# Performance work log

Hardware: AMD Instinct MI355X
Metric: run time of the kernel (lower is better)

Reference implementation:

```python
import jax, jax.numpy as jnp
import numpy as np

INTERVAL = 0.5  # voxel_size_ratio
N_RAYS = 131072
M_SAMPLES = 8388608  # ~64 samples per ray on average
ALPHA_INIT = 0.01


def setup_inputs() -> dict:
    key = jax.random.key(0)
    k1, k2, k3 = jax.random.split(key, 3)
    density = jax.random.normal(k1, (M_SAMPLES,), jnp.float32)
    rgb_feat = jax.random.normal(k2, (M_SAMPLES, 3), jnp.float32)  # raw k0 colors
    # act_shift buffer: log(1/(1-alpha_init) - 1)
    shift = jnp.array([np.log(1.0 / (1.0 - ALPHA_INIT) - 1.0)], jnp.float32)
    # sorted ray ids (samples along each ray are contiguous, near->far)
    ray_id = jnp.sort(jax.random.randint(k3, (M_SAMPLES,), 0, N_RAYS)).astype(jnp.int32)
    return {"density": density, "rgb_feat": rgb_feat, "shift": shift,
            "ray_id": ray_id, "N": N_RAYS}


def reference(density, rgb_feat, shift, ray_id, N):
    # Raw2Alpha: alpha = 1 - (1 + exp(density + shift))^(-interval)
    #          = 1 - exp(-softplus(density + shift) * interval)
    sp = jax.nn.softplus(density + shift[0])
    log1ma = -sp * INTERVAL            # log(1 - alpha), exact
    alpha = 1.0 - jnp.exp(log1ma)

    # Alphas2Weights: per-ray exclusive cumulative product of (1 - alpha)
    # done in log space with a segmented exclusive cumsum.
    seg_tot = jax.ops.segment_sum(log1ma, ray_id, num_segments=N)   # [N] log prod per ray
    seg_excl = jnp.cumsum(seg_tot) - seg_tot                        # log prod of previous rays
    within_excl = jnp.cumsum(log1ma) - log1ma - seg_excl[ray_id]    # exclusive within segment
    T = jnp.exp(within_excl)          # transmittance before each sample
    weights = alpha * T               # [M]
    alphainv_last = jnp.exp(seg_tot)  # [N] leftover transmittance per ray

    # composite colors per ray + white-ish background via alphainv_last
    rgb = jax.nn.sigmoid(rgb_feat)
    rgb_marched = jax.ops.segment_sum(weights[:, None] * rgb, ray_id, num_segments=N)
    out = rgb_marched + alphainv_last[:, None]   # [N, 3]
    return weights, alphainv_last, out
```

## Files before the change

kernel.cpp:

```cpp
#include <hip/hip_runtime.h>

#define INTERVAL 0.5f

__device__ __forceinline__ float cheap_softplus(float x) {
    float e = __expf(-fabsf(x));
    return fmaxf(x, 0.0f) + __logf(1.0f + e);
}

__device__ __forceinline__ float fast_sigmoid(float x) {
    return 1.0f / (1.0f + __expf(-x));
}

#define DPP_ADD(x, ctrl, rmask)                                               \
    do {                                                                      \
        int _s = __builtin_amdgcn_update_dpp(0, __float_as_int(x), (ctrl),    \
                                             (rmask), 0xf, true);             \
        (x) += __int_as_float(_s);                                            \
    } while (0)

__device__ __forceinline__ float wave_inclusive_scan(float x) {
    DPP_ADD(x, 0x111, 0xf);
    DPP_ADD(x, 0x112, 0xf);
    DPP_ADD(x, 0x114, 0xf);
    DPP_ADD(x, 0x118, 0xf);
    DPP_ADD(x, 0x142, 0xa);
    DPP_ADD(x, 0x143, 0xc);
    return x;
}

__device__ __forceinline__ float bcast_lane63(float x) {
    return __int_as_float(__builtin_amdgcn_readlane(__float_as_int(x), 63));
}

__global__ __launch_bounds__(256) void seg_starts_kernel(
    const int* __restrict__ ray_id, int M, int N, int* __restrict__ starts)
{
    const int i = blockIdx.x * blockDim.x + threadIdx.x;
    if (i >= M) return;
    const int cur  = ray_id[i];
    const int prev = (i == 0) ? -1 : ray_id[i - 1];
    for (int r = prev + 1; r <= cur; ++r) starts[r] = i;
    if (i == M - 1) {
        for (int r = cur + 1; r <= N; ++r) starts[r] = M;
    }
}

__global__ __launch_bounds__(256) void favor_render_kernel(
    const float* __restrict__ density,
    const float* __restrict__ rgb_feat,
    const float* __restrict__ shift,
    const int*   __restrict__ starts,
    int M, int N,
    float* __restrict__ weights,
    float* __restrict__ alphainv_last,
    float* __restrict__ out3)
{
    const int wave = (blockIdx.x * blockDim.x + threadIdx.x) >> 6;
    const int t    = threadIdx.x & 63;
    if (wave >= N) return;
    const int ray = wave;

    const int start = starts[ray];
    const int end   = starts[ray + 1];

    const float sh = shift[0];

    float carry = 0.0f;
    float acc0 = 0.0f, acc1 = 0.0f, acc2 = 0.0f;

    for (int base = start; base < end; base += 128) {
        const int i0 = base + t;
        const int i1 = i0 + 64;
        const bool v0 = (i0 < end);
        const bool v1 = (i1 < end);
        const bool any1 = (base + 64) < end;

        const int c0 = min(i0, end - 1);
        float d0 = density[c0];
        float r0 = rgb_feat[3 * c0 + 0];
        float g0 = rgb_feat[3 * c0 + 1];
        float b0 = rgb_feat[3 * c0 + 2];

        float d1 = 0.0f, r1 = 0.0f, g1 = 0.0f, b1 = 0.0f;
        if (any1) {
            const int c1 = min(i1, end - 1);
            d1 = density[c1];
            r1 = rgb_feat[3 * c1 + 0];
            g1 = rgb_feat[3 * c1 + 1];
            b1 = rgb_feat[3 * c1 + 2];
        }

        const float l0  = -INTERVAL * cheap_softplus(d0 + sh);
        const float l1  = -INTERVAL * cheap_softplus(d1 + sh);
        const float lv0 = v0 ? l0 : 0.0f;
        const float lv1 = v1 ? l1 : 0.0f;

        const float s0 = wave_inclusive_scan(lv0);
        const float s1 = wave_inclusive_scan(lv1);
        const float tot0 = bcast_lane63(s0);
        const float tot1 = bcast_lane63(s1);

        const float e0 = carry + (s0 - lv0);
        const float e1 = carry + tot0 + (s1 - lv1);

        const float w0 = __expf(e0) - __expf(e0 + l0);
        const float w1 = __expf(e1) - __expf(e1 + l1);

        if (v0) {
            weights[i0] = w0;
            acc0 += w0 * fast_sigmoid(r0);
            acc1 += w0 * fast_sigmoid(g0);
            acc2 += w0 * fast_sigmoid(b0);
        }
        if (v1) {
            weights[i1] = w1;
            acc0 += w1 * fast_sigmoid(r1);
            acc1 += w1 * fast_sigmoid(g1);
            acc2 += w1 * fast_sigmoid(b1);
        }
        carry += tot0 + tot1;
    }

    const float s_acc0 = bcast_lane63(wave_inclusive_scan(acc0));
    const float s_acc1 = bcast_lane63(wave_inclusive_scan(acc1));
    const float s_acc2 = bcast_lane63(wave_inclusive_scan(acc2));

    if (t == 0) {
        const float ainv = __expf(carry);
        alphainv_last[ray] = ainv;
        out3[3 * ray + 0] = s_acc0 + ainv;
        out3[3 * ray + 1] = s_acc1 + ainv;
        out3[3 * ray + 2] = s_acc2 + ainv;
    }
}

extern "C" void kernel_launch(void* const* d_in, const int* in_sizes, int n_in,
                              void* d_out, int out_size, void* d_ws, size_t ws_size,
                              hipStream_t stream) {
    const float* density  = (const float*)d_in[0];
    const float* rgb_feat = (const float*)d_in[1];
    const float* shift    = (const float*)d_in[2];
    const int*   ray_id   = (const int*)d_in[3];

    const int M = in_sizes[0];
    const int N = (out_size - M) / 4;

    float* weights       = (float*)d_out;
    float* alphainv_last = weights + M;
    float* out3          = alphainv_last + N;

    const int block = 256;
    int* starts = (int*)d_ws;

    const int grid_starts = (M + block - 1) / block;
    seg_starts_kernel<<<grid_starts, block, 0, stream>>>(ray_id, M, N, starts);

    const int grid_render = (N * 64 + block - 1) / block;
    favor_render_kernel<<<grid_render, block, 0, stream>>>(
        density, rgb_feat, shift, starts, M, N,
        weights, alphainv_last, out3);
}
```

Before: 223.6 us.

## Compute transmittance as multiplicative scan using rsqrt alpha, vectorize segment-start search

Replaces the log-space softplus/exp pipeline with the closed form 1-alpha = (1+exp(x))^-0.5, computed via one exp and an rsq, and scans transmittance multiplicatively with DPP multiplies. Weights become T*(u*a-1), which removes the log and extra exps per sample. The segment-start kernel now reads ray ids as int4, so each thread handles four samples. Repeated products may underflow on long rays and lose precision compared with summing logs.

Result: no change. 220.8 us (-1.2%).

```diff
diff --git a/kernel.cpp b/kernel.cpp
--- a/kernel.cpp
+++ b/kernel.cpp
@@ -1,14 +1,8 @@
 #include <hip/hip_runtime.h>
 
-#define INTERVAL 0.5f
-
-__device__ __forceinline__ float cheap_softplus(float x) {
-    float e = __expf(-fabsf(x));
-    return fmaxf(x, 0.0f) + __logf(1.0f + e);
-}
 
 __device__ __forceinline__ float fast_sigmoid(float x) {
-    return 1.0f / (1.0f + __expf(-x));
+    return __builtin_amdgcn_rcpf(1.0f + __expf(-x));
 }
 
 #define DPP_ADD(x, ctrl, rmask)                                               \
@@ -18,7 +12,14 @@
         (x) += __int_as_float(_s);                                            \
     } while (0)
 
-__device__ __forceinline__ float wave_inclusive_scan(float x) {
+#define DPP_MUL(x, ctrl, rmask)                                               \
+    do {                                                                      \
+        int _s = __builtin_amdgcn_update_dpp(0x3f800000, __float_as_int(x),   \
+                                             (ctrl), (rmask), 0xf, false);    \
+        (x) *= __int_as_float(_s);                                            \
+    } while (0)
+
+__device__ __forceinline__ float wave_scan_add(float x) {
     DPP_ADD(x, 0x111, 0xf);
     DPP_ADD(x, 0x112, 0xf);
     DPP_ADD(x, 0x114, 0xf);
@@ -28,20 +29,41 @@
     return x;
 }
 
+__device__ __forceinline__ float wave_scan_mul(float x) {
+    DPP_MUL(x, 0x111, 0xf);
+    DPP_MUL(x, 0x112, 0xf);
+    DPP_MUL(x, 0x114, 0xf);
+    DPP_MUL(x, 0x118, 0xf);
+    DPP_MUL(x, 0x142, 0xa);
+    DPP_MUL(x, 0x143, 0xc);
+    return x;
+}
+
 __device__ __forceinline__ float bcast_lane63(float x) {
     return __int_as_float(__builtin_amdgcn_readlane(__float_as_int(x), 63));
 }
 
-__global__ __launch_bounds__(256) void seg_starts_kernel(
-    const int* __restrict__ ray_id, int M, int N, int* __restrict__ starts)
+__global__ __launch_bounds__(256) void seg_starts4_kernel(
+    const int4* __restrict__ ray4, int M4, int M, int N,
+    const int* __restrict__ ray_id, int* __restrict__ starts)
 {
     const int i = blockIdx.x * blockDim.x + threadIdx.x;
-    if (i >= M) return;
-    const int cur  = ray_id[i];
-    const int prev = (i == 0) ? -1 : ray_id[i - 1];
-    for (int r = prev + 1; r <= cur; ++r) starts[r] = i;
-    if (i == M - 1) {
-        for (int r = cur + 1; r <= N; ++r) starts[r] = M;
+    if (i >= M4) return;
+    const int4 v = ray4[i];
+    const int prev = (i == 0) ? -1 : ray_id[4 * i - 1];
+    const int base = 4 * i;
+    for (int r = prev + 1; r <= v.x; ++r) starts[r] = base;
+    for (int r = v.x + 1;  r <= v.y; ++r) starts[r] = base + 1;
+    for (int r = v.y + 1;  r <= v.z; ++r) starts[r] = base + 2;
+    for (int r = v.z + 1;  r <= v.w; ++r) starts[r] = base + 3;
+    if (i == M4 - 1) {
+        int last = v.w;
+        for (int j = 4 * M4; j < M; ++j) {
+            const int cur = ray_id[j];
+            for (int r = last + 1; r <= cur; ++r) starts[r] = j;
+            last = cur;
+        }
+        for (int r = last + 1; r <= N; ++r) starts[r] = M;
     }
 }
 
@@ -65,7 +87,7 @@
 
     const float sh = shift[0];
 
-    float carry = 0.0f;
+    float carryT = 1.0f;
     float acc0 = 0.0f, acc1 = 0.0f, acc2 = 0.0f;
 
     for (int base = start; base < end; base += 128) {
@@ -76,11 +98,10 @@
         const bool any1 = (base + 64) < end;
 
         const int c0 = min(i0, end - 1);
-        float d0 = density[c0];
-        float r0 = rgb_feat[3 * c0 + 0];
-        float g0 = rgb_feat[3 * c0 + 1];
-        float b0 = rgb_feat[3 * c0 + 2];
-
+        const float d0 = density[c0];
+        const float r0 = rgb_feat[3 * c0 + 0];
+        const float g0 = rgb_feat[3 * c0 + 1];
+        const float b0 = rgb_feat[3 * c0 + 2];
         float d1 = 0.0f, r1 = 0.0f, g1 = 0.0f, b1 = 0.0f;
         if (any1) {
             const int c1 = min(i1, end - 1);
@@ -90,43 +111,46 @@
             b1 = rgb_feat[3 * c1 + 2];
         }
 
-        const float l0  = -INTERVAL * cheap_softplus(d0 + sh);
-        const float l1  = -INTERVAL * cheap_softplus(d1 + sh);
-        const float lv0 = v0 ? l0 : 0.0f;
-        const float lv1 = v1 ? l1 : 0.0f;
-
-        const float s0 = wave_inclusive_scan(lv0);
-        const float s1 = wave_inclusive_scan(lv1);
+        const float u0 = 1.0f + __expf(d0 + sh);
+        const float a0 = __builtin_amdgcn_rsqf(u0);
+        const float m0 = v0 ? a0 : 1.0f;
+        const float s0 = wave_scan_mul(m0);
         const float tot0 = bcast_lane63(s0);
-        const float tot1 = bcast_lane63(s1);
-
-        const float e0 = carry + (s0 - lv0);
-        const float e1 = carry + tot0 + (s1 - lv1);
-
-        const float w0 = __expf(e0) - __expf(e0 + l0);
-        const float w1 = __expf(e1) - __expf(e1 + l1);
-
+        const float Ti0  = carryT * s0;
+        const float w0   = Ti0 * (u0 * a0 - 1.0f);
         if (v0) {
             weights[i0] = w0;
             acc0 += w0 * fast_sigmoid(r0);
             acc1 += w0 * fast_sigmoid(g0);
             acc2 += w0 * fast_sigmoid(b0);
         }
-        if (v1) {
-            weights[i1] = w1;
-            acc0 += w1 * fast_sigmoid(r1);
-            acc1 += w1 * fast_sigmoid(g1);
-            acc2 += w1 * fast_sigmoid(b1);
+
+        if (any1) {
+            const float u1 = 1.0f + __expf(d1 + sh);
+            const float a1 = __builtin_amdgcn_rsqf(u1);
+            const float m1 = v1 ? a1 : 1.0f;
+            const float s1 = wave_scan_mul(m1);
+            const float tot1 = bcast_lane63(s1);
+            const float Ti1  = carryT * tot0 * s1;
+            const float w1   = Ti1 * (u1 * a1 - 1.0f);
+            if (v1) {
+                weights[i1] = w1;
+                acc0 += w1 * fast_sigmoid(r1);
+                acc1 += w1 * fast_sigmoid(g1);
+                acc2 += w1 * fast_sigmoid(b1);
+            }
+            carryT *= tot0 * tot1;
+        } else {
+            carryT *= tot0;
         }
-        carry += tot0 + tot1;
     }
 
-    const float s_acc0 = bcast_lane63(wave_inclusive_scan(acc0));
-    const float s_acc1 = bcast_lane63(wave_inclusive_scan(acc1));
-    const float s_acc2 = bcast_lane63(wave_inclusive_scan(acc2));
+    const float s_acc0 = bcast_lane63(wave_scan_add(acc0));
+    const float s_acc1 = bcast_lane63(wave_scan_add(acc1));
+    const float s_acc2 = bcast_lane63(wave_scan_add(acc2));
 
     if (t == 0) {
-        const float ainv = __expf(carry);
+        const float ainv = carryT;
         alphainv_last[ray] = ainv;
         out3[3 * ray + 0] = s_acc0 + ainv;
         out3[3 * ray + 1] = s_acc1 + ainv;
@@ -152,8 +176,10 @@
     const int block = 256;
     int* starts = (int*)d_ws;
 
-    const int grid_starts = (M + block - 1) / block;
-    seg_starts_kernel<<<grid_starts, block, 0, stream>>>(ray_id, M, N, starts);
+    const int M4 = M >> 2;
+    const int grid_starts = (M4 + block - 1) / block;
+    seg_starts4_kernel<<<grid_starts, block, 0, stream>>>(
+        (const int4*)ray_id, M4, M, N, ray_id, starts);
 
     const int grid_render = (N * 64 + block - 1) / block;
     favor_render_kernel<<<grid_render, block, 0, stream>>>(
```
